# Optimization experiments

Measured on AMD Instinct MI355X. Metric: run time of the kernel, lower is better.

The kernel has to match this reference:

```python
import jax, jax.numpy as jnp
import numpy as np

DIM = 2048
H = 16
D = DIM // H  # 128
B = 2
L = 2048


def rms_norm(x, scale):
    # torch: x.float(); rrms = rsqrt(mean(x^2)+1e-6); (x*rrms).to(dtype)*scale
    xf = x.astype(jnp.float32)
    rrms = jax.lax.rsqrt(jnp.mean(xf * xf, axis=-1, keepdims=True) + 1e-6)
    return (xf * rrms).astype(x.dtype) * scale


def apply_rope(xq, xk, pe):
    # pe: [1,1,L,D//2,2,2]; q/k: [B,H,L,D]
    xq_ = xq.astype(jnp.float32).reshape(*xq.shape[:-1], -1, 1, 2)
    xk_ = xk.astype(jnp.float32).reshape(*xk.shape[:-1], -1, 1, 2)
    xq_out = pe[..., 0] * xq_[..., 0] + pe[..., 1] * xq_[..., 1]
    xk_out = pe[..., 0] * xk_[..., 0] + pe[..., 1] * xk_[..., 1]
    return xq_out.reshape(xq.shape).astype(xq.dtype), xk_out.reshape(xk.shape).astype(xk.dtype)


def setup_inputs() -> dict:
    key = jax.random.key(0)
    ks = jax.random.split(key, 8)
    x = jax.random.normal(ks[0], (B, L, DIM), dtype=jnp.float32)
    pos_enc = jax.random.normal(ks[1], (1, 1, L, D // 2, 2, 2), dtype=jnp.float32)
    qkv_w = jax.random.normal(ks[2], (3 * DIM, DIM), dtype=jnp.float32) * (1.0 / np.sqrt(DIM))
    q_scale = jnp.ones((D,), dtype=jnp.float32)
    k_scale = jnp.ones((D,), dtype=jnp.float32)
    proj_w = jax.random.normal(ks[3], (DIM, DIM), dtype=jnp.float32) * (1.0 / np.sqrt(DIM))
    proj_b = jnp.zeros((DIM,), dtype=jnp.float32)
    return {"x": x, "pos_enc": pos_enc, "qkv_w": qkv_w, "q_scale": q_scale,
            "k_scale": k_scale, "proj_w": proj_w, "proj_b": proj_b}


def reference(x, pos_enc, qkv_w, q_scale, k_scale, proj_w, proj_b):
    b, l, dim = x.shape
    qkv = jnp.einsum('bld,ed->ble', x, qkv_w)  # [B,L,3*DIM]
    qkv = qkv.reshape(b, l, 3, H, D).transpose(2, 0, 3, 1, 4)  # [3,B,H,L,D]
    q, k, v = qkv[0], qkv[1], qkv[2]
    q = rms_norm(q, q_scale).astype(v.dtype)
    k = rms_norm(k, k_scale).astype(v.dtype)
    q, k = apply_rope(q, k, pos_enc)
    scale = 1.0 / np.sqrt(D)
    scores = jnp.einsum('bhqd,bhkd->bhqk', q, k) * scale
    probs = jax.nn.softmax(scores, axis=-1)
    o = jnp.einsum('bhqk,bhkd->bhqd', probs, v)  # [B,H,L,D]
    o = o.transpose(0, 2, 1, 3).reshape(b, l, dim)  # B H L D -> B L (H D)
    return jnp.einsum('bld,ed->ble', o, proj_w) + proj_b
```

## Files before the change

kernel.cpp:

```cpp
#include <hip/hip_runtime.h>
#include <stdint.h>

typedef unsigned short u16;
typedef short bf16x8 __attribute__((ext_vector_type(8)));
typedef float f32x4 __attribute__((ext_vector_type(4)));

#define B_   2
#define L_   2048
#define DIM_ 2048
#define H_   16
#define D_   128
#define E3_  6144
#define ML_  4096

__device__ __forceinline__ u16 f2b(float f) {
  union { float f; unsigned u; } v; v.f = f;
  return (u16)((v.u + 0x7FFFu + ((v.u >> 16) & 1u)) >> 16);
}
__device__ __forceinline__ float b2f(u16 h) {
  union { unsigned u; float f; } v; v.u = ((unsigned)h) << 16; return v.f;
}

__device__ __forceinline__ void gl_lds16(const void* g, void* l) {
  __builtin_amdgcn_global_load_lds((const __attribute__((address_space(1))) void*)g,
                                   (__attribute__((address_space(3))) void*)l, 16, 0, 0);
}

__global__ __launch_bounds__(256) void cvt_kernel(const float* __restrict__ in,
                                                  u16* __restrict__ out, int n4) {
  int i = blockIdx.x * 256 + threadIdx.x;
  int stride = gridDim.x * 256;
  for (; i < n4; i += stride) {
    float4 v = reinterpret_cast<const float4*>(in)[i];
    ushort4 o = make_ushort4(f2b(v.x), f2b(v.y), f2b(v.z), f2b(v.w));
    reinterpret_cast<ushort4*>(out)[i] = o;
  }
}

template<int OUTF32>
__global__ __launch_bounds__(256, 2) void gemm_bt(
    const u16* __restrict__ A, const u16* __restrict__ Bm,
    u16* __restrict__ Cb, float* __restrict__ Cf, const float* __restrict__ bias,
    int M, int N, int K) {
  __shared__ __align__(16) u16 As[128 * 32];
  __shared__ __align__(16) u16 Bs[128 * 32];
  const int tid = threadIdx.x;
  const int w = tid >> 6;
  const int g = (tid >> 4) & 3, r = tid & 15;
  const int wr = w >> 1, wc = w & 1;
  const long row0 = (long)blockIdx.y * 128, col0 = (long)blockIdx.x * 128;

  const f32x4 fz = {0.f, 0.f, 0.f, 0.f};
  f32x4 acc[4][4];
#pragma unroll
  for (int m = 0; m < 4; ++m)
#pragma unroll
    for (int n = 0; n < 4; ++n) acc[m][n] = fz;

  for (int k0 = 0; k0 < K; k0 += 32) {
#pragma unroll
    for (int it = 0; it < 2; ++it) {
      int c = it * 256 + tid;
      gl_lds16(A + (row0 + (c >> 2)) * (long)K + k0 + ((c & 3) << 3),
               (char*)As + ((it * 256 + (w << 6)) << 4));
      gl_lds16(Bm + (col0 + (c >> 2)) * (long)K + k0 + ((c & 3) << 3),
               (char*)Bs + ((it * 256 + (w << 6)) << 4));
    }
    __syncthreads();
    bf16x8 af[4], bfr[4];
#pragma unroll
    for (int m = 0; m < 4; ++m)
      af[m] = *reinterpret_cast<const bf16x8*>(As + (wr * 64 + m * 16 + r) * 32 + g * 8);
#pragma unroll
    for (int n = 0; n < 4; ++n)
      bfr[n] = *reinterpret_cast<const bf16x8*>(Bs + (wc * 64 + n * 16 + r) * 32 + g * 8);
#pragma unroll
    for (int m = 0; m < 4; ++m)
#pragma unroll
      for (int n = 0; n < 4; ++n)
        acc[m][n] = __builtin_amdgcn_mfma_f32_16x16x32_bf16(af[m], bfr[n], acc[m][n], 0, 0, 0);
    __syncthreads();
  }

#pragma unroll
  for (int m = 0; m < 4; ++m)
#pragma unroll
    for (int n = 0; n < 4; ++n)
#pragma unroll
      for (int j = 0; j < 4; ++j) {
        long rr = row0 + wr * 64 + m * 16 + g * 4 + j;
        long cc = col0 + wc * 64 + n * 16 + r;
        if constexpr (OUTF32) {
          Cf[rr * N + cc] = acc[m][n][j] + bias[cc];
        } else {
          Cb[rr * N + cc] = f2b(acc[m][n][j]);
        }
      }
}

__global__ __launch_bounds__(256) void normrope_kernel(
    const u16* __restrict__ qkv, const float* __restrict__ pe,
    const float* __restrict__ qsc, const float* __restrict__ ksc,
    u16* __restrict__ Qo, u16* __restrict__ Ko) {
  const int w = threadIdx.x >> 6, ln = threadIdx.x & 63;
  const int idx = blockIdx.x * 4 + w;
  const int h = idx & 15, bl = idx >> 4;
  const int l = bl & (L_ - 1), b = bl >> 11;
  const u16* base = qkv + (long)bl * E3_ + h * D_;
  const float4 pv = *reinterpret_cast<const float4*>(pe + ((long)l * 64 + ln) * 4);
  const long obase = (((long)(b * H_ + h)) * L_ + l) * D_ + 2 * ln;
  {
    unsigned qv = *reinterpret_cast<const unsigned*>(base + 2 * ln);
    float x0 = b2f((u16)qv), x1 = b2f((u16)(qv >> 16));
    float ss = x0 * x0 + x1 * x1;
#pragma unroll
    for (int msk = 1; msk < 64; msk <<= 1) ss += __shfl_xor(ss, msk);
    float rr = rsqrtf(ss * (1.0f / 128.0f) + 1e-6f);
    float y0 = x0 * rr * qsc[2 * ln], y1 = x1 * rr * qsc[2 * ln + 1];
    float o0 = pv.x * y0 + pv.y * y1, o1 = pv.z * y0 + pv.w * y1;
    *reinterpret_cast<unsigned*>(Qo + obase) = (unsigned)f2b(o0) | ((unsigned)f2b(o1) << 16);
  }
  {
    unsigned kv = *reinterpret_cast<const unsigned*>(base + DIM_ + 2 * ln);
    float x0 = b2f((u16)kv), x1 = b2f((u16)(kv >> 16));
    float ss = x0 * x0 + x1 * x1;
#pragma unroll
    for (int msk = 1; msk < 64; msk <<= 1) ss += __shfl_xor(ss, msk);
    float rr = rsqrtf(ss * (1.0f / 128.0f) + 1e-6f);
    float y0 = x0 * rr * ksc[2 * ln], y1 = x1 * rr * ksc[2 * ln + 1];
    float o0 = pv.x * y0 + pv.y * y1, o1 = pv.z * y0 + pv.w * y1;
    *reinterpret_cast<unsigned*>(Ko + obase) = (unsigned)f2b(o0) | ((unsigned)f2b(o1) << 16);
  }
}

__global__ __launch_bounds__(256) void vtrans_kernel(const u16* __restrict__ qkv,
                                                     u16* __restrict__ VT) {
  __shared__ u16 t[64][132];
  const int tid = threadIdx.x;
  const int bh = blockIdx.x >> 5, lt = blockIdx.x & 31;
  const int b = bh >> 4, h = bh & 15;
  const int l0 = lt << 6;
  const u16* src = qkv + ((long)(b * L_ + l0)) * E3_ + 2 * DIM_ + h * D_;
#pragma unroll
  for (int i = 0; i < 32; ++i) {
    int o = i * 256 + tid;
    int lr = o >> 7, d = o & 127;
    t[lr][d] = src[(long)lr * E3_ + d];
  }
  __syncthreads();
  u16* dst = VT + (long)bh * (D_ * L_) + l0;
#pragma unroll
  for (int i = 0; i < 32; ++i) {
    int o = i * 256 + tid;
    int d = o >> 6, lr = o & 63;
    dst[(long)d * L_ + lr] = t[lr][d];
  }
}

__global__ __launch_bounds__(256, 2) void flash_kernel(
    const u16* __restrict__ Qg, const u16* __restrict__ Kg,
    const u16* __restrict__ Vt, u16* __restrict__ Og) {
  __shared__ __align__(16) u16 Ks[2][64 * 128];
  __shared__ __align__(16) u16 Vs[2][128 * 64];
  __shared__ __align__(16) u16 Ps[128 * 64];
  const int tid = threadIdx.x, w = tid >> 6;
  const int g = (tid >> 4) & 3, r = tid & 15;
  const int bh = blockIdx.y, q0 = blockIdx.x * 128;
  const int b = bh >> 4, h = bh & 15;
  const u16* Qb = Qg + (long)bh * (L_ * D_);
  const u16* Kb = Kg + (long)bh * (L_ * D_);
  const u16* Vb = Vt + (long)bh * (L_ * D_);
  char* PsB = (char*)Ps;
  const float sc = 0.08838834764831845f;

  bf16x8 qf[2][4];
#pragma unroll
  for (int m = 0; m < 2; ++m)
#pragma unroll
    for (int t = 0; t < 4; ++t)
      qf[m][t] = *reinterpret_cast<const bf16x8*>(
          Qb + (long)(q0 + w * 32 + m * 16 + r) * D_ + t * 32 + g * 8);

  const f32x4 fz = {0.f, 0.f, 0.f, 0.f};
  f32x4 oacc[2][8];
  f32x4 mrun[2], lrun[2];
#pragma unroll
  for (int m = 0; m < 2; ++m) {
    mrun[m] = (f32x4){-3.0e38f, -3.0e38f, -3.0e38f, -3.0e38f};
    lrun[m] = fz;
#pragma unroll
    for (int n = 0; n < 8; ++n) oacc[m][n] = fz;
  }

  auto stage = [&](int buf, int kt) {
    const int kk0 = kt * 64;
    const u16* Ksrc = Kb + (long)kk0 * D_;
    char* KsB = (char*)Ks[buf];
    char* VsB = (char*)Vs[buf];
#pragma unroll
    for (int it = 0; it < 4; ++it) {
      int c = it * 256 + tid;
      int pb = c << 4;
      int krow = pb >> 8;
      int klb = (pb & 255) ^ ((krow & 7) << 4);
      gl_lds16(Ksrc + (long)krow * D_ + (klb >> 1), KsB + ((it * 256 + (w << 6)) << 4));
      int vrow = pb >> 7;
      int vlb = (pb & 127) ^ ((vrow & 7) << 4);
      gl_lds16(Vb + (long)vrow * L_ + kk0 + (vlb >> 1), VsB + ((it * 256 + (w << 6)) << 4));
    }
  };

  stage(0, 0);
  asm volatile("s_waitcnt vmcnt(0)" ::: "memory");
  __builtin_amdgcn_s_barrier();

  for (int kt = 0; kt < 32; ++kt) {
    const int cur = kt & 1;
    if (kt + 1 < 32) stage(cur ^ 1, kt + 1);
    const char* KsB = (const char*)Ks[cur];
    const char* VsB = (const char*)Vs[cur];

    f32x4 s[2][4];
#pragma unroll
    for (int m = 0; m < 2; ++m)
#pragma unroll
      for (int n = 0; n < 4; ++n) s[m][n] = fz;
    __builtin_amdgcn_s_setprio(1);
#pragma unroll
    for (int t = 0; t < 4; ++t) {
#pragma unroll
      for (int n = 0; n < 4; ++n) {
        int kr = n * 16 + r;
        bf16x8 kf = *reinterpret_cast<const bf16x8*>(
            KsB + ((kr << 8) | ((t * 64 + g * 16) ^ ((kr & 7) << 4))));
#pragma unroll
        for (int m = 0; m < 2; ++m)
          s[m][n] = __builtin_amdgcn_mfma_f32_16x16x32_bf16(qf[m][t], kf, s[m][n], 0, 0, 0);
      }
    }
    __builtin_amdgcn_s_setprio(0);

#pragma unroll
    for (int m = 0; m < 2; ++m) {
      f32x4 rmx = s[m][0];
#pragma unroll
      for (int n = 1; n < 4; ++n)
#pragma unroll
        for (int j = 0; j < 4; ++j) rmx[j] = fmaxf(rmx[j], s[m][n][j]);
#pragma unroll
      for (int j = 0; j < 4; ++j) {
#pragma unroll
        for (int msk = 1; msk < 16; msk <<= 1)
          rmx[j] = fmaxf(rmx[j], __shfl_xor(rmx[j], msk));
      }
      float growth = rmx[0] * sc - mrun[m][0];
#pragma unroll
      for (int j = 1; j < 4; ++j) growth = fmaxf(growth, rmx[j] * sc - mrun[m][j]);
      if (!__all(growth <= 8.0f)) {
#pragma unroll
        for (int j = 0; j < 4; ++j) {
          float mnew = fmaxf(mrun[m][j], rmx[j] * sc);
          float corr = __expf(mrun[m][j] - mnew);
          mrun[m][j] = mnew;
          lrun[m][j] *= corr;
#pragma unroll
          for (int n = 0; n < 8; ++n) oacc[m][n][j] *= corr;
        }
      }
      f32x4 rsum = fz;
#pragma unroll
      for (int n = 0; n < 4; ++n) {
#pragma unroll
        for (int j = 0; j < 4; ++j) {
          float p = __expf(s[m][n][j] * sc - mrun[m][j]);
          rsum[j] += p;
          int ql = w * 32 + m * 16 + g * 4 + j;
          int col = n * 16 + r;
          *reinterpret_cast<u16*>(PsB + ((ql << 7) | ((col << 1) ^ ((ql & 7) << 4)))) = f2b(p);
        }
      }
#pragma unroll
      for (int j = 0; j < 4; ++j) {
#pragma unroll
        for (int msk = 1; msk < 16; msk <<= 1) rsum[j] += __shfl_xor(rsum[j], msk);
        lrun[m][j] += rsum[j];
      }
    }

    __builtin_amdgcn_s_setprio(1);
#pragma unroll
    for (int t = 0; t < 2; ++t) {
      bf16x8 pf[2];
#pragma unroll
      for (int m = 0; m < 2; ++m) {
        int pr = w * 32 + m * 16 + r;
        pf[m] = *reinterpret_cast<const bf16x8*>(
            PsB + ((pr << 7) | ((t * 64 + g * 16) ^ ((pr & 7) << 4))));
      }
#pragma unroll
      for (int n = 0; n < 8; ++n) {
        int vr = n * 16 + r;
        bf16x8 vf = *reinterpret_cast<const bf16x8*>(
            VsB + ((vr << 7) | ((t * 64 + g * 16) ^ ((vr & 7) << 4))));
#pragma unroll
        for (int m = 0; m < 2; ++m)
          oacc[m][n] = __builtin_amdgcn_mfma_f32_16x16x32_bf16(pf[m], vf, oacc[m][n], 0, 0, 0);
      }
    }
    __builtin_amdgcn_s_setprio(0);

    asm volatile("s_waitcnt vmcnt(0)" ::: "memory");
    __builtin_amdgcn_s_barrier();
  }

#pragma unroll
  for (int m = 0; m < 2; ++m) {
    f32x4 inv;
#pragma unroll
    for (int j = 0; j < 4; ++j) inv[j] = 1.0f / lrun[m][j];
#pragma unroll
    for (int n = 0; n < 8; ++n)
#pragma unroll
      for (int j = 0; j < 4; ++j) {
        int ql = w * 32 + m * 16 + g * 4 + j;
        int col = n * 16 + r;
        Og[((long)(b * L_) + q0 + ql) * DIM_ + h * D_ + col] = f2b(oacc[m][n][j] * inv[j]);
      }
  }
}

extern "C" void kernel_launch(void* const* d_in, const int* in_sizes, int n_in,
                              void* d_out, int out_size, void* d_ws, size_t ws_size,
                              hipStream_t stream) {
  const float* x    = (const float*)d_in[0];
  const float* pe   = (const float*)d_in[1];
  const float* qkvw = (const float*)d_in[2];
  const float* qsc  = (const float*)d_in[3];
  const float* ksc  = (const float*)d_in[4];
  const float* pw   = (const float*)d_in[5];
  const float* pb   = (const float*)d_in[6];
  float* out = (float*)d_out;

  u16* ws_x   = (u16*)d_ws;
  u16* ws_w1  = ws_x   + (size_t)ML_ * DIM_;
  u16* ws_w2  = ws_w1  + (size_t)E3_ * DIM_;
  u16* ws_qkv = ws_w2  + (size_t)DIM_ * DIM_;
  u16* ws_q   = ws_qkv + (size_t)ML_ * E3_;
  u16* ws_k   = ws_q   + (size_t)ML_ * DIM_;
  u16* ws_vt  = ws_k   + (size_t)ML_ * DIM_;
  u16* ws_o   = ws_vt  + (size_t)ML_ * DIM_;

  cvt_kernel<<<2048, 256, 0, stream>>>(x, ws_x, ML_ * DIM_ / 4);
  cvt_kernel<<<2048, 256, 0, stream>>>(qkvw, ws_w1, E3_ * DIM_ / 4);
  cvt_kernel<<<2048, 256, 0, stream>>>(pw, ws_w2, DIM_ * DIM_ / 4);

  gemm_bt<0><<<dim3(E3_ / 128, ML_ / 128), 256, 0, stream>>>(
      ws_x, ws_w1, ws_qkv, nullptr, nullptr, ML_, E3_, DIM_);
  normrope_kernel<<<(B_ * L_ * H_) / 4, 256, 0, stream>>>(ws_qkv, pe, qsc, ksc, ws_q, ws_k);
  vtrans_kernel<<<B_ * H_ * (L_ / 64), 256, 0, stream>>>(ws_qkv, ws_vt);
  flash_kernel<<<dim3(L_ / 128, B_ * H_), 256, 0, stream>>>(ws_q, ws_k, ws_vt, ws_o);
  gemm_bt<1><<<dim3(DIM_ / 128, ML_ / 128), 256, 0, stream>>>(
      ws_o, ws_w2, nullptr, out, pb, ML_, DIM_, DIM_);
}
```

Baseline: 483.1 us.

## Split flash attention work across 8 waves with 16 query rows each

The flash kernel moves from 256 to 512 threads per block, with each wave owning 16 query rows instead of 32. The staging loop is adjusted so all threads cooperatively load K/V tiles. This aims to raise wave-level parallelism and latency hiding per CU and to cut register pressure. The cost is less reuse of each K/V LDS fragment, so LDS read traffic per MFMA doubles.

Result: no change. 477.8 us (-1.1%).

```diff
diff --git a/kernel.cpp b/kernel.cpp
--- a/kernel.cpp
+++ b/kernel.cpp
@@ -157,7 +157,7 @@
   }
 }
 
-__global__ __launch_bounds__(256, 2) void flash_kernel(
+__global__ __launch_bounds__(512, 2) void flash_kernel(
     const u16* __restrict__ Qg, const u16* __restrict__ Kg,
     const u16* __restrict__ Vt, u16* __restrict__ Og) {
   __shared__ __align__(16) u16 Ks[2][64 * 128];
@@ -172,25 +172,20 @@
   const u16* Vb = Vt + (long)bh * (L_ * D_);
   char* PsB = (char*)Ps;
   const float sc = 0.08838834764831845f;
-
-  bf16x8 qf[2][4];
-#pragma unroll
-  for (int m = 0; m < 2; ++m)
-#pragma unroll
-    for (int t = 0; t < 4; ++t)
-      qf[m][t] = *reinterpret_cast<const bf16x8*>(
-          Qb + (long)(q0 + w * 32 + m * 16 + r) * D_ + t * 32 + g * 8);
+  const int qrow = w * 16;
+
+  bf16x8 qf[4];
+#pragma unroll
+  for (int t = 0; t < 4; ++t)
+    qf[t] = *reinterpret_cast<const bf16x8*>(
+        Qb + (long)(q0 + qrow + r) * D_ + t * 32 + g * 8);
 
   const f32x4 fz = {0.f, 0.f, 0.f, 0.f};
-  f32x4 oacc[2][8];
-  f32x4 mrun[2], lrun[2];
-#pragma unroll
-  for (int m = 0; m < 2; ++m) {
-    mrun[m] = (f32x4){-3.0e38f, -3.0e38f, -3.0e38f, -3.0e38f};
-    lrun[m] = fz;
-#pragma unroll
-    for (int n = 0; n < 8; ++n) oacc[m][n] = fz;
-  }
+  f32x4 oacc[8];
+  f32x4 mrun = (f32x4){-3.0e38f, -3.0e38f, -3.0e38f, -3.0e38f};
+  f32x4 lrun = fz;
+#pragma unroll
+  for (int n = 0; n < 8; ++n) oacc[n] = fz;
 
   auto stage = [&](int buf, int kt) {
     const int kk0 = kt * 64;
@@ -198,15 +193,15 @@
     char* KsB = (char*)Ks[buf];
     char* VsB = (char*)Vs[buf];
 #pragma unroll
-    for (int it = 0; it < 4; ++it) {
-      int c = it * 256 + tid;
+    for (int it = 0; it < 2; ++it) {
+      int c = it * 512 + tid;
       int pb = c << 4;
       int krow = pb >> 8;
       int klb = (pb & 255) ^ ((krow & 7) << 4);
-      gl_lds16(Ksrc + (long)krow * D_ + (klb >> 1), KsB + ((it * 256 + (w << 6)) << 4));
+      gl_lds16(Ksrc + (long)krow * D_ + (klb >> 1), KsB + ((it * 512 + (w << 6)) << 4));
       int vrow = pb >> 7;
       int vlb = (pb & 127) ^ ((vrow & 7) << 4);
-      gl_lds16(Vb + (long)vrow * L_ + kk0 + (vlb >> 1), VsB + ((it * 256 + (w << 6)) << 4));
+      gl_lds16(Vb + (long)vrow * L_ + kk0 + (vlb >> 1), VsB + ((it * 512 + (w << 6)) << 4));
     }
   };
 
@@ -220,11 +215,9 @@
     const char* KsB = (const char*)Ks[cur];
     const char* VsB = (const char*)Vs[cur];
 
-    f32x4 s[2][4];
-#pragma unroll
-    for (int m = 0; m < 2; ++m)
-#pragma unroll
-      for (int n = 0; n < 4; ++n) s[m][n] = fz;
+    f32x4 s[4];
+#pragma unroll
+    for (int n = 0; n < 4; ++n) s[n] = fz;
     __builtin_amdgcn_s_setprio(1);
 #pragma unroll
     for (int t = 0; t < 4; ++t) {
@@ -233,38 +226,35 @@
         int kr = n * 16 + r;
         bf16x8 kf = *reinterpret_cast<const bf16x8*>(
             KsB + ((kr << 8) | ((t * 64 + g * 16) ^ ((kr & 7) << 4))));
-#pragma unroll
-        for (int m = 0; m < 2; ++m)
-          s[m][n] = __builtin_amdgcn_mfma_f32_16x16x32_bf16(qf[m][t], kf, s[m][n], 0, 0, 0);
+        s[n] = __builtin_amdgcn_mfma_f32_16x16x32_bf16(qf[t], kf, s[n], 0, 0, 0);
       }
     }
     __builtin_amdgcn_s_setprio(0);
 
-#pragma unroll
-    for (int m = 0; m < 2; ++m) {
-      f32x4 rmx = s[m][0];
+    {
+      f32x4 rmx = s[0];
 #pragma unroll
       for (int n = 1; n < 4; ++n)
 #pragma unroll
-        for (int j = 0; j < 4; ++j) rmx[j] = fmaxf(rmx[j], s[m][n][j]);
+        for (int j = 0; j < 4; ++j) rmx[j] = fmaxf(rmx[j], s[n][j]);
 #pragma unroll
       for (int j = 0; j < 4; ++j) {
 #pragma unroll
         for (int msk = 1; msk < 16; msk <<= 1)
           rmx[j] = fmaxf(rmx[j], __shfl_xor(rmx[j], msk));
       }
-      float growth = rmx[0] * sc - mrun[m][0];
-#pragma unroll
-      for (int j = 1; j < 4; ++j) growth = fmaxf(growth, rmx[j] * sc - mrun[m][j]);
+      float growth = rmx[0] * sc - mrun[0];
+#pragma unroll
+      for (int j = 1; j < 4; ++j) growth = fmaxf(growth, rmx[j] * sc - mrun[j]);
       if (!__all(growth <= 8.0f)) {
 #pragma unroll
         for (int j = 0; j < 4; ++j) {
-          float mnew = fmaxf(mrun[m][j], rmx[j] * sc);
-          float corr = __expf(mrun[m][j] - mnew);
-          mrun[m][j] = mnew;
-          lrun[m][j] *= corr;
-#pragma unroll
-          for (int n = 0; n < 8; ++n) oacc[m][n][j] *= corr;
+          float mnew = fmaxf(mrun[j], rmx[j] * sc);
+          float corr = __expf(mrun[j] - mnew);
+          mrun[j] = mnew;
+          lrun[j] *= corr;
+#pragma unroll
+          for (int n = 0; n < 8; ++n) oacc[n][j] *= corr;
         }
       }
       f32x4 rsum = fz;
@@ -272,9 +262,9 @@
       for (int n = 0; n < 4; ++n) {
 #pragma unroll
         for (int j = 0; j < 4; ++j) {
-          float p = __expf(s[m][n][j] * sc - mrun[m][j]);
+          float p = __expf(s[n][j] * sc - mrun[j]);
           rsum[j] += p;
-          int ql = w * 32 + m * 16 + g * 4 + j;
+          int ql = qrow + g * 4 + j;
           int col = n * 16 + r;
           *reinterpret_cast<u16*>(PsB + ((ql << 7) | ((col << 1) ^ ((ql & 7) << 4)))) = f2b(p);
         }
@@ -283,28 +273,22 @@
       for (int j = 0; j < 4; ++j) {
 #pragma unroll
         for (int msk = 1; msk < 16; msk <<= 1) rsum[j] += __shfl_xor(rsum[j], msk);
-        lrun[m][j] += rsum[j];
+        lrun[j] += rsum[j];
       }
     }
 
     __builtin_amdgcn_s_setprio(1);
 #pragma unroll
     for (int t = 0; t < 2; ++t) {
-      bf16x8 pf[2];
-#pragma unroll
-      for (int m = 0; m < 2; ++m) {
-        int pr = w * 32 + m * 16 + r;
-        pf[m] = *reinterpret_cast<const bf16x8*>(
-            PsB + ((pr << 7) | ((t * 64 + g * 16) ^ ((pr & 7) << 4))));
-      }
+      int pr = qrow + r;
+      bf16x8 pf = *reinterpret_cast<const bf16x8*>(
+          PsB + ((pr << 7) | ((t * 64 + g * 16) ^ ((pr & 7) << 4))));
 #pragma unroll
       for (int n = 0; n < 8; ++n) {
         int vr = n * 16 + r;
         bf16x8 vf = *reinterpret_cast<const bf16x8*>(
             VsB + ((vr << 7) | ((t * 64 + g * 16) ^ ((vr & 7) << 4))));
-#pragma unroll
-        for (int m = 0; m < 2; ++m)
-          oacc[m][n] = __builtin_amdgcn_mfma_f32_16x16x32_bf16(pf[m], vf, oacc[m][n], 0, 0, 0);
+        oacc[n] = __builtin_amdgcn_mfma_f32_16x16x32_bf16(pf, vf, oacc[n], 0, 0, 0);
       }
     }
     __builtin_amdgcn_s_setprio(0);
@@ -313,18 +297,17 @@
     __builtin_amdgcn_s_barrier();
   }
 
-#pragma unroll
-  for (int m = 0; m < 2; ++m) {
+  {
     f32x4 inv;
 #pragma unroll
-    for (int j = 0; j < 4; ++j) inv[j] = 1.0f / lrun[m][j];
+    for (int j = 0; j < 4; ++j) inv[j] = 1.0f / lrun[j];
 #pragma unroll
     for (int n = 0; n < 8; ++n)
 #pragma unroll
       for (int j = 0; j < 4; ++j) {
-        int ql = w * 32 + m * 16 + g * 4 + j;
+        int ql = qrow + g * 4 + j;
         int col = n * 16 + r;
-        Og[((long)(b * L_) + q0 + ql) * DIM_ + h * D_ + col] = f2b(oacc[m][n][j] * inv[j]);
+        Og[((long)(b * L_) + q0 + ql) * DIM_ + h * D_ + col] = f2b(oacc[n][j] * inv[j]);
       }
   }
 }
@@ -358,7 +341,7 @@
       ws_x, ws_w1, ws_qkv, nullptr, nullptr, ML_, E3_, DIM_);
   normrope_kernel<<<(B_ * L_ * H_) / 4, 256, 0, stream>>>(ws_qkv, pe, qsc, ksc, ws_q, ws_k);
   vtrans_kernel<<<B_ * H_ * (L_ / 64), 256, 0, stream>>>(ws_qkv, ws_vt);
-  flash_kernel<<<dim3(L_ / 128, B_ * H_), 256, 0, stream>>>(ws_q, ws_k, ws_vt, ws_o);
+  flash_kernel<<<dim3(L_ / 128, B_ * H_), 512, 0, stream>>>(ws_q, ws_k, ws_vt, ws_o);
   gemm_bt<1><<<dim3(DIM_ / 128, ML_ / 128), 256, 0, stream>>>(
       ws_o, ws_w2, nullptr, out, pb, ML_, DIM_, DIM_);
 }
```
